# Performance work log

Hardware: AMD Instinct MI355X
Metric: run time of the kernel (lower is better)

The kernel has to match this reference:

```python
import jax, jax.numpy as jnp
import numpy as np

L = 16384      # sequence length
D_IN = 512     # d_input
D_H = 1024     # d_hidden
D_OUT = 512    # d_output
R_MIN = 0.0
R_MAX = 0.99
MAX_PHASE = np.pi


def setup_inputs() -> dict:
    key = jax.random.key(0)
    k_nu, k_th, k_x, k_bre, k_bim, k_cre, k_cim, k_d = jax.random.split(key, 8)
    # nu_init with parametrization='exp'
    u_nu = jax.random.uniform(k_nu, (D_H,), dtype=jnp.float32)
    nu = jnp.sqrt(u_nu * (R_MAX ** 2 - R_MIN ** 2) + R_MIN ** 2)
    u_theta = jax.random.uniform(k_th, (D_H,), dtype=jnp.float32, minval=-MAX_PHASE, maxval=MAX_PHASE)
    theta = jnp.mod(u_theta, 2 * jnp.pi)
    lamb = jnp.stack([jnp.log(-jnp.log(nu)), jnp.log(theta)], axis=0)  # [2, D_H]
    # gamma_init with parametrization='exp': nu = exp(-exp(lamb[0]))
    nu_eff = jnp.exp(-jnp.exp(lamb[0]))
    gamma = jnp.log(jnp.sqrt(1.0 - jnp.abs(nu_eff) ** 2))  # [D_H]
    # matrix_init: normal / sqrt(shape[0])
    B_re = jax.random.normal(k_bre, (D_H, D_IN), dtype=jnp.float32) / jnp.sqrt(D_H)
    B_im = jax.random.normal(k_bim, (D_H, D_IN), dtype=jnp.float32) / jnp.sqrt(D_H)
    C_re = jax.random.normal(k_cre, (D_OUT, D_H), dtype=jnp.float32) / jnp.sqrt(D_OUT)
    C_im = jax.random.normal(k_cim, (D_OUT, D_H), dtype=jnp.float32) / jnp.sqrt(D_OUT)
    D = jax.random.normal(k_d, (D_OUT, D_IN), dtype=jnp.float32) / jnp.sqrt(D_OUT)
    inputs = jax.random.normal(k_x, (L, D_IN), dtype=jnp.float32)
    return {"inputs": inputs, "lamb": lamb, "gamma": gamma,
            "B_re": B_re, "B_im": B_im, "C_re": C_re, "C_im": C_im, "D": D}


def _binary_operator_diag(q_i, q_j):
    A_i, b_i = q_i
    A_j, b_j = q_j
    return (A_j * A_i, A_j * b_i + b_j)


def reference(inputs, lamb, gamma, B_re, B_im, C_re, C_im, D):
    # parametrization='exp': lambda = exp(-exp(nu_log) + i*exp(theta_log))
    diag_lambda = jnp.exp(-jnp.exp(lamb[0]) + 1j * jnp.exp(lamb[1]))  # [D_H] complex64
    # which_gamma='learned', exp param: scale rows of B by exp(gamma)
    B_norm = jnp.exp(gamma)[:, None] * (B_re + 1j * B_im)             # [D_H, D_IN]
    # Bu_t = B_norm @ x_t for all t, as one GEMM: [L, D_H] complex
    Bu = inputs.astype(B_norm.dtype) @ B_norm.T
    Lambda_elements = jnp.broadcast_to(diag_lambda[None, :], Bu.shape)
    # diagonal linear recurrence h_t = lambda*h_{t-1} + Bu_t via parallel scan
    _, h = jax.lax.associative_scan(_binary_operator_diag, (Lambda_elements, Bu))
    C = C_re + 1j * C_im
    # y_t = Re[C h_t] + D x_t
    outputs = jnp.real(h @ C.T) + inputs @ D.T  # [L, D_OUT]
    return outputs
```

## Files before the change

### kernel.cpp

```cpp
#include <hip/hip_runtime.h>

__device__ __forceinline__ unsigned short f2b(float f) {
    unsigned int u = __builtin_bit_cast(unsigned int, f);
    unsigned int r = (u + 0x7FFFu + ((u >> 16) & 1u)) >> 16;
    return (unsigned short)r;
}
__device__ __forceinline__ float b2f(unsigned short s) {
    unsigned int u = ((unsigned int)s) << 16;
    return __builtin_bit_cast(float, u);
}

typedef __attribute__((ext_vector_type(8))) short short8;
typedef __attribute__((ext_vector_type(4))) float float4v;

#define GLD16(g, l) __builtin_amdgcn_global_load_lds(                          \
    (const __attribute__((address_space(1))) unsigned int*)(g),                \
    (__attribute__((address_space(3))) unsigned int*)(l), 16, 0, 0)

#define WAIT_VMN(n)  __builtin_amdgcn_s_waitcnt(0x0F70 | (n))
#define WAIT_LGKM0() __builtin_amdgcn_s_waitcnt(0xC07F)
#define SB()         __builtin_amdgcn_sched_barrier(0)
#define BAR()        __builtin_amdgcn_s_barrier()

#define SEQLEN 16384
#define NCHUNK 512
#define TCHUNK 32
#define LDH 2560

__global__ void prep_all(const float* __restrict__ x,
                         const float* __restrict__ B_re, const float* __restrict__ B_im,
                         const float* __restrict__ gamma,
                         const float* __restrict__ C_re, const float* __restrict__ C_im,
                         const float* __restrict__ Dm,
                         unsigned short* __restrict__ Hcat,
                         unsigned short* __restrict__ Bcat,
                         unsigned short* __restrict__ CW) {
    int b = blockIdx.x;
    if (b < 8192) {
        int id = b * 256 + threadIdx.x;
        int t = id >> 7;
        int k4 = (id & 127) << 2;
        float4 v = *(const float4*)(x + (long)t * 512 + k4);
        ushort4 o;
        o.x = f2b(v.x); o.y = f2b(v.y); o.z = f2b(v.z); o.w = f2b(v.w);
        *(ushort4*)(Hcat + (long)t * LDH + 2048 + k4) = o;
    } else if (b < 9216) {
        int id = (b - 8192) * 256 + threadIdx.x;
        int n = id >> 7;
        int k4 = (id & 127) << 2;
        const float* src = (n < 1024) ? (B_re + (long)n * 512) : (B_im + (long)(n - 1024) * 512);
        float g = expf(gamma[n & 1023]);
        float4 v = *(const float4*)(src + k4);
        ushort4 o;
        o.x = f2b(v.x * g); o.y = f2b(v.y * g); o.z = f2b(v.z * g); o.w = f2b(v.w * g);
        *(ushort4*)(Bcat + (long)n * 512 + k4) = o;
    } else {
        int id = (b - 9216) * 256 + threadIdx.x;
        int o = id / 640;
        int j4 = (id - o * 640) << 2;
        float4 v; float sgn = 1.0f;
        if (j4 < 1024) {
            v = *(const float4*)(C_re + (long)o * 1024 + j4);
        } else if (j4 < 2048) {
            v = *(const float4*)(C_im + (long)o * 1024 + (j4 - 1024));
            sgn = -1.0f;
        } else {
            v = *(const float4*)(Dm + (long)o * 512 + (j4 - 2048));
        }
        ushort4 w;
        w.x = f2b(v.x * sgn); w.y = f2b(v.y * sgn); w.z = f2b(v.z * sgn); w.w = f2b(v.w * sgn);
        *(ushort4*)(CW + (long)o * 2560 + j4) = w;
    }
}

template <int MREP, bool OUT_BF16>
__launch_bounds__(512, 2)
__global__ void gemm_8p(const unsigned short* __restrict__ A, int lda,
                        const unsigned short* __restrict__ B, int ldb,
                        void* __restrict__ Cout, int ldc, int Ktot,
                        int nbx_shift) {
    constexpr int BM  = MREP * 32;
    constexpr int ASH = BM * 64;
    constexpr int NA  = BM / 64;
    constexpr int GPT = NA + 4;
    __shared__ unsigned short sm[2][ASH + 16384] __attribute__((aligned(16)));

    const int tid  = threadIdx.x;
    const int lane = tid & 63;
    const int wid  = tid >> 6;
    const int wr   = wid >> 2;
    const int wc   = wid & 3;

    const int bid = blockIdx.x;
    const int xcd = bid & 7;
    const int g   = bid >> 3;
    const int bx  = g & ((1 << nbx_shift) - 1);
    const int by  = xcd * (gridDim.x >> (3 + nbx_shift)) + (g >> nbx_shift);
    const long m0 = (long)by * BM;
    const long n0 = (long)bx * 256;

    const int sr = lane >> 3;
    const int sc = ((lane & 7) ^ sr) << 3;
    const unsigned short* Agl = A + (m0 + sr) * (long)lda + sc;
    const unsigned short* Bgl = B + (n0 + sr) * (long)ldb + sc;

    const int fr = lane & 15;
    const int x7 = fr & 7;
    const int k0off = (((lane >> 4)    ) ^ x7) << 3;
    const int k1off = (((lane >> 4) + 4) ^ x7) << 3;

    float4v acc[MREP][4] = {};
    short8 fa[4][2];
    short8 fb[4][2];

    auto stageB = [&](unsigned short* buf, long kt) {
        unsigned short* ldsB = buf + ASH + wid * 512;
        const unsigned short* gB = Bgl + kt;
#pragma unroll
        for (int i = 0; i < 4; i++)
            GLD16(gB + (long)(8 * (wid + 8 * i)) * ldb, ldsB + i * 4096);
    };
    auto stageA = [&](unsigned short* buf, long kt) {
        unsigned short* ldsA = buf + wid * 512;
        const unsigned short* gA = Agl + kt;
#pragma unroll
        for (int i = 0; i < NA; i++)
            GLD16(gA + (long)(8 * (wid + 8 * i)) * lda, ldsA + i * 4096);
    };
    auto ldB = [&](const unsigned short* buf, int nbase) {
#pragma unroll
        for (int j = 0; j < 2; j++) {
            const unsigned short* p = buf + ASH + (wc * 64 + (nbase + j) * 16 + fr) * 64;
            fb[nbase + j][0] = *(const short8*)(p + k0off);
            fb[nbase + j][1] = *(const short8*)(p + k1off);
        }
    };

    const int nk = Ktot >> 6;

    stageB(sm[0], 0);  stageA(sm[0], 0);
    stageB(sm[1], 64); stageA(sm[1], 64);
    WAIT_VMN(GPT);
    SB(); BAR(); SB();

    if constexpr (MREP == 8) {
        auto ldA = [&](const unsigned short* buf, int mbase) {
#pragma unroll
            for (int i = 0; i < 4; i++) {
                const unsigned short* p = buf + (wr * 128 + (mbase + i) * 16 + fr) * 64;
                fa[i][0] = *(const short8*)(p + k0off);
                fa[i][1] = *(const short8*)(p + k1off);
            }
        };
        auto mfmaQ = [&](int mbase, int nbase) {
            __builtin_amdgcn_s_setprio(1);
#pragma unroll
            for (int i = 0; i < 4; i++)
#pragma unroll
                for (int j = 0; j < 2; j++) {
                    acc[mbase + i][nbase + j] = __builtin_amdgcn_mfma_f32_16x16x32_bf16(
                        fa[i][0], fb[nbase + j][0], acc[mbase + i][nbase + j], 0, 0, 0);
                    acc[mbase + i][nbase + j] = __builtin_amdgcn_mfma_f32_16x16x32_bf16(
                        fa[i][1], fb[nbase + j][1], acc[mbase + i][nbase + j], 0, 0, 0);
                }
            __builtin_amdgcn_s_setprio(0);
        };
        for (int t = 0; t < nk; ++t) {
            unsigned short* cur = sm[t & 1];
            const bool st = (t + 2 < nk);
            const long kt2 = (long)(t + 2) * 64;
            ldA(cur, 0); ldB(cur, 0);
            SB(); BAR(); SB();
            mfmaQ(0, 0);
            SB(); BAR(); SB();
            ldB(cur, 2);
            SB(); BAR(); SB();
            mfmaQ(0, 2);
            SB(); BAR(); SB();
            if (st) stageB(cur, kt2);
            ldA(cur, 4);
            SB(); BAR(); SB();
            mfmaQ(4, 0);
            SB(); BAR(); SB();
            if (st) stageA(cur, kt2);
            SB();
            mfmaQ(4, 2);
            if (st)              WAIT_VMN(GPT);
            else if (t + 1 < nk) WAIT_VMN(0);
            SB(); BAR(); SB();
        }
    } else {
        auto ldAall = [&](const unsigned short* buf) {
#pragma unroll
            for (int i = 0; i < 4; i++) {
                const unsigned short* p = buf + (wr * 64 + i * 16 + fr) * 64;
                fa[i][0] = *(const short8*)(p + k0off);
                fa[i][1] = *(const short8*)(p + k1off);
            }
        };
        auto mfmaN2 = [&](int nbase) {
            __builtin_amdgcn_s_setprio(1);
#pragma unroll
            for (int i = 0; i < 4; i++)
#pragma unroll
                for (int j = 0; j < 2; j++) {
                    acc[i][nbase + j] = __builtin_amdgcn_mfma_f32_16x16x32_bf16(
                        fa[i][0], fb[nbase + j][0], acc[i][nbase + j], 0, 0, 0);
                    acc[i][nbase + j] = __builtin_amdgcn_mfma_f32_16x16x32_bf16(
                        fa[i][1], fb[nbase + j][1], acc[i][nbase + j], 0, 0, 0);
                }
            __builtin_amdgcn_s_setprio(0);
        };
        for (int t = 0; t < nk; ++t) {
            unsigned short* cur = sm[t & 1];
            const bool st = (t + 2 < nk);
            const long kt2 = (long)(t + 2) * 64;
            ldAall(cur); ldB(cur, 0);
            SB(); BAR(); SB();
            mfmaN2(0);
            SB(); BAR(); SB();
            ldB(cur, 2);
            WAIT_LGKM0();
            SB(); BAR(); SB();
            if (st) { stageB(cur, kt2); stageA(cur, kt2); }
            SB();
            mfmaN2(2);
            if (st)              WAIT_VMN(GPT);
            else if (t + 1 < nk) WAIT_VMN(0);
            SB(); BAR(); SB();
        }
    }

    const int er = (lane >> 4) * 4;
    const int ec = lane & 15;
#pragma unroll
    for (int mi = 0; mi < MREP; mi++) {
#pragma unroll
        for (int r = 0; r < 4; r++) {
            long grow = m0 + wr * (BM / 2) + mi * 16 + er + r;
#pragma unroll
            for (int nj = 0; nj < 4; nj++) {
                long gcol = n0 + wc * 64 + nj * 16 + ec;
                float v = acc[mi][nj][r];
                if (OUT_BF16)
                    ((unsigned short*)Cout)[grow * ldc + gcol] = f2b(v);
                else
                    ((float*)Cout)[grow * ldc + gcol] = v;
            }
        }
    }
}

__global__ void scan_ends(const unsigned short* __restrict__ Hcat,
                          const float* __restrict__ lamb,
                          float* __restrict__ E) {
    const int chunk = blockIdx.x;
    const int ch = threadIdx.x << 2;
    float lre[4], lim[4];
#pragma unroll
    for (int i = 0; i < 4; i++) {
        float nu = expf(-expf(lamb[ch + i]));
        float th = expf(lamb[1024 + ch + i]);
        lre[i] = nu * cosf(th);
        lim[i] = nu * sinf(th);
    }
    float hr[4] = {0, 0, 0, 0}, hi[4] = {0, 0, 0, 0};
    const unsigned short* base = Hcat + (long)chunk * TCHUNK * LDH + ch;
#pragma unroll 4
    for (int t = 0; t < TCHUNK; t++) {
        ushort4 br = *(const ushort4*)(base + (long)t * LDH);
        ushort4 bi = *(const ushort4*)(base + (long)t * LDH + 1024);
        float brf[4] = {b2f(br.x), b2f(br.y), b2f(br.z), b2f(br.w)};
        float bif[4] = {b2f(bi.x), b2f(bi.y), b2f(bi.z), b2f(bi.w)};
#pragma unroll
        for (int i = 0; i < 4; i++) {
            float nr = fmaf(lre[i], hr[i], fmaf(-lim[i], hi[i], brf[i]));
            float ni = fmaf(lre[i], hi[i], fmaf(lim[i], hr[i], bif[i]));
            hr[i] = nr; hi[i] = ni;
        }
    }
    float* Ec = E + (long)chunk * 2048 + ch;
#pragma unroll
    for (int i = 0; i < 4; i++) {
        Ec[i] = hr[i];
        Ec[1024 + i] = hi[i];
    }
}

__global__ void carry(const float* __restrict__ lamb, const float* __restrict__ E,
                      float* __restrict__ Kc) {
    const int lane = threadIdx.x & 63;
    const int ch = blockIdx.x * 4 + (threadIdx.x >> 6);
    double nu = exp(-exp((double)lamb[ch]));
    double th = exp((double)lamb[1024 + ch]);
    double lr = nu * cos(th), li = nu * sin(th);
#pragma unroll
    for (int i = 0; i < 5; i++) {
        double rr = lr * lr - li * li;
        double ii = 2.0 * lr * li;
        lr = rr; li = ii;
    }
    const float tre = (float)lr, tim = (float)li;
    double ar = lr, ai = li;
#pragma unroll
    for (int i = 0; i < 3; i++) {
        double rr = ar * ar - ai * ai;
        double ii = 2.0 * ar * ai;
        ar = rr; ai = ii;
    }
    float Ar = (float)ar, Ai = (float)ai;

    const int c0 = lane * 8;
    float er[8], ei[8];
#pragma unroll
    for (int j = 0; j < 8; j++) {
        er[j] = E[(long)(c0 + j) * 2048 + ch];
        ei[j] = E[(long)(c0 + j) * 2048 + 1024 + ch];
    }
    float hr = 0.0f, hi = 0.0f;
#pragma unroll
    for (int j = 0; j < 8; j++) {
        float nr = fmaf(tre, hr, fmaf(-tim, hi, er[j]));
        float ni = fmaf(tre, hi, fmaf(tim, hr, ei[j]));
        hr = nr; hi = ni;
    }
#pragma unroll
    for (int o = 1; o < 64; o <<= 1) {
        float pr = __shfl_up(hr, o);
        float pi = __shfl_up(hi, o);
        float qr = __shfl_up(Ar, o);
        float qi = __shfl_up(Ai, o);
        if (lane >= o) {
            float nr = fmaf(Ar, pr, fmaf(-Ai, pi, hr));
            float ni = fmaf(Ar, pi, fmaf(Ai, pr, hi));
            hr = nr; hi = ni;
            float nar = Ar * qr - Ai * qi;
            float nai = Ar * qi + Ai * qr;
            Ar = nar; Ai = nai;
        }
    }
    float sr = __shfl_up(hr, 1);
    float si = __shfl_up(hi, 1);
    if (lane == 0) { sr = 0.0f; si = 0.0f; }
#pragma unroll
    for (int j = 0; j < 8; j++) {
        Kc[(long)(c0 + j) * 2048 + ch] = sr;
        Kc[(long)(c0 + j) * 2048 + 1024 + ch] = si;
        float nr = fmaf(tre, sr, fmaf(-tim, si, er[j]));
        float ni = fmaf(tre, si, fmaf(tim, sr, ei[j]));
        sr = nr; si = ni;
    }
}

__global__ void scan_apply(unsigned short* __restrict__ Hcat,
                           const float* __restrict__ lamb,
                           const float* __restrict__ Kc) {
    const int chunk = blockIdx.x;
    const int ch = threadIdx.x << 2;
    float lre[4], lim[4];
#pragma unroll
    for (int i = 0; i < 4; i++) {
        float nu = expf(-expf(lamb[ch + i]));
        float th = expf(lamb[1024 + ch + i]);
        lre[i] = nu * cosf(th);
        lim[i] = nu * sinf(th);
    }
    float hr[4], hi[4];
#pragma unroll
    for (int i = 0; i < 4; i++) {
        hr[i] = Kc[(long)chunk * 2048 + ch + i];
        hi[i] = Kc[(long)chunk * 2048 + 1024 + ch + i];
    }
    unsigned short* base = Hcat + (long)chunk * TCHUNK * LDH + ch;
#pragma unroll 4
    for (int t = 0; t < TCHUNK; t++) {
        ushort4 br = *(const ushort4*)(base + (long)t * LDH);
        ushort4 bi = *(const ushort4*)(base + (long)t * LDH + 1024);
        float brf[4] = {b2f(br.x), b2f(br.y), b2f(br.z), b2f(br.w)};
        float bif[4] = {b2f(bi.x), b2f(bi.y), b2f(bi.z), b2f(bi.w)};
#pragma unroll
        for (int i = 0; i < 4; i++) {
            float nr = fmaf(lre[i], hr[i], fmaf(-lim[i], hi[i], brf[i]));
            float ni = fmaf(lre[i], hi[i], fmaf(lim[i], hr[i], bif[i]));
            hr[i] = nr; hi[i] = ni;
        }
        ushort4 orv, oiv;
        orv.x = f2b(hr[0]); orv.y = f2b(hr[1]); orv.z = f2b(hr[2]); orv.w = f2b(hr[3]);
        oiv.x = f2b(hi[0]); oiv.y = f2b(hi[1]); oiv.z = f2b(hi[2]); oiv.w = f2b(hi[3]);
        *(ushort4*)(base + (long)t * LDH) = orv;
        *(ushort4*)(base + (long)t * LDH + 1024) = oiv;
    }
}

extern "C" void kernel_launch(void* const* d_in, const int* in_sizes, int n_in,
                              void* d_out, int out_size, void* d_ws, size_t ws_size,
                              hipStream_t stream) {
    const float* x     = (const float*)d_in[0];
    const float* lamb  = (const float*)d_in[1];
    const float* gamma = (const float*)d_in[2];
    const float* B_re  = (const float*)d_in[3];
    const float* B_im  = (const float*)d_in[4];
    const float* C_re  = (const float*)d_in[5];
    const float* C_im  = (const float*)d_in[6];
    const float* Dm    = (const float*)d_in[7];

    char* ws = (char*)d_ws;
    unsigned short* Hcat = (unsigned short*)ws;
    float* E  = (float*)(ws + 83886080);
    float* Kc = E + (long)NCHUNK * 2048;
    unsigned short* Bcat = (unsigned short*)((char*)Kc + 4194304);
    unsigned short* CW   = Bcat + (long)2048 * 512;

    prep_all<<<10496, 256, 0, stream>>>(x, B_re, B_im, gamma, C_re, C_im, Dm, Hcat, Bcat, CW);
    gemm_8p<8, true><<<512, 512, 0, stream>>>(Hcat + 2048, LDH, Bcat, 512, Hcat, LDH, 512,
                                              3);
    scan_ends<<<NCHUNK, 256, 0, stream>>>(Hcat, lamb, E);
    carry<<<256, 256, 0, stream>>>(lamb, E, Kc);
    scan_apply<<<NCHUNK, 256, 0, stream>>>(Hcat, lamb, Kc);
    gemm_8p<4, false><<<256, 512, 0, stream>>>(Hcat, LDH, CW, 2560, (float*)d_out, 512, 2560,
                                               1);
}
```

Before: 242.1 us.

## Replace 8-wave GEMM with 4-wave 256x128 tile, K=32 triple-buffered pipeline

Replaces the templated 8-wave GEMM with a single 4-wave kernel that uses 256x128 output tiles, a K step of 32, and three rotating LDS buffers with a new XOR swizzle. Both GEMMs now launch with 256 threads: the first on 1024 blocks and the second on 256 blocks with 256x128 tiles. The aim is a deeper prefetch pipeline and more MFMA work per wave with fewer barriers per tile. In exchange, each K iteration is shorter, so barriers are relatively more frequent. The output GEMM also gets fewer waves in total, which may leave the device underfilled.

```diff
diff --git a/kernel.cpp b/kernel.cpp
--- a/kernel.cpp
+++ b/kernel.cpp
@@ -18,7 +18,6 @@
     (__attribute__((address_space(3))) unsigned int*)(l), 16, 0, 0)
 
 #define WAIT_VMN(n)  __builtin_amdgcn_s_waitcnt(0x0F70 | (n))
-#define WAIT_LGKM0() __builtin_amdgcn_s_waitcnt(0xC07F)
 #define SB()         __builtin_amdgcn_sched_barrier(0)
 #define BAR()        __builtin_amdgcn_s_barrier()
 
@@ -73,171 +72,100 @@
     }
 }
 
-template <int MREP, bool OUT_BF16>
-__launch_bounds__(512, 2)
-__global__ void gemm_8p(const unsigned short* __restrict__ A, int lda,
+template <bool OUT_BF16>
+__launch_bounds__(256, 2)
+__global__ void gemm_w4(const unsigned short* __restrict__ A, int lda,
                         const unsigned short* __restrict__ B, int ldb,
                         void* __restrict__ Cout, int ldc, int Ktot,
                         int nbx_shift) {
-    constexpr int BM  = MREP * 32;
-    constexpr int ASH = BM * 64;
-    constexpr int NA  = BM / 64;
-    constexpr int GPT = NA + 4;
-    __shared__ unsigned short sm[2][ASH + 16384] __attribute__((aligned(16)));
-
+    __shared__ unsigned short sm[3][12288] __attribute__((aligned(16)));
     const int tid  = threadIdx.x;
     const int lane = tid & 63;
     const int wid  = tid >> 6;
-    const int wr   = wid >> 2;
-    const int wc   = wid & 3;
+    const int wr   = wid >> 1;
+    const int wc   = wid & 1;
 
     const int bid = blockIdx.x;
     const int xcd = bid & 7;
     const int g   = bid >> 3;
     const int bx  = g & ((1 << nbx_shift) - 1);
     const int by  = xcd * (gridDim.x >> (3 + nbx_shift)) + (g >> nbx_shift);
-    const long m0 = (long)by * BM;
-    const long n0 = (long)bx * 256;
-
-    const int sr = lane >> 3;
-    const int sc = ((lane & 7) ^ sr) << 3;
+    const long m0 = (long)by * 256;
+    const long n0 = (long)bx * 128;
+
+    const int sr = lane >> 2;
+    const int sc = (((lane & 3) ^ ((lane >> 3) & 3)) << 3);
     const unsigned short* Agl = A + (m0 + sr) * (long)lda + sc;
     const unsigned short* Bgl = B + (n0 + sr) * (long)ldb + sc;
 
-    const int fr = lane & 15;
-    const int x7 = fr & 7;
-    const int k0off = (((lane >> 4)    ) ^ x7) << 3;
-    const int k1off = (((lane >> 4) + 4) ^ x7) << 3;
-
-    float4v acc[MREP][4] = {};
-    short8 fa[4][2];
-    short8 fb[4][2];
-
-    auto stageB = [&](unsigned short* buf, long kt) {
-        unsigned short* ldsB = buf + ASH + wid * 512;
-        const unsigned short* gB = Bgl + kt;
+    const int fr   = lane & 15;
+    const int koff = (((lane >> 4) ^ ((fr >> 1) & 3)) << 3);
+
+    float4v acc[8][4] = {};
+    short8 fa[8], fb[4];
+
+    auto stage = [&](unsigned short* buf, long kt) {
 #pragma unroll
         for (int i = 0; i < 4; i++)
-            GLD16(gB + (long)(8 * (wid + 8 * i)) * ldb, ldsB + i * 4096);
+            GLD16(Agl + (long)(wid * 64 + i * 16) * lda + kt, buf + (wid * 4 + i) * 512);
+#pragma unroll
+        for (int j = 0; j < 2; j++)
+            GLD16(Bgl + (long)(wid * 32 + j * 16) * ldb + kt, buf + 8192 + (wid * 2 + j) * 512);
     };
-    auto stageA = [&](unsigned short* buf, long kt) {
-        unsigned short* ldsA = buf + wid * 512;
-        const unsigned short* gA = Agl + kt;
-#pragma unroll
-        for (int i = 0; i < NA; i++)
-            GLD16(gA + (long)(8 * (wid + 8 * i)) * lda, ldsA + i * 4096);
+    auto ldAall = [&](const unsigned short* buf) {
+#pragma unroll
+        for (int i = 0; i < 8; i++)
+            fa[i] = *(const short8*)(buf + (wr * 128 + i * 16 + fr) * 32 + koff);
     };
-    auto ldB = [&](const unsigned short* buf, int nbase) {
-#pragma unroll
-        for (int j = 0; j < 2; j++) {
-            const unsigned short* p = buf + ASH + (wc * 64 + (nbase + j) * 16 + fr) * 64;
-            fb[nbase + j][0] = *(const short8*)(p + k0off);
-            fb[nbase + j][1] = *(const short8*)(p + k1off);
-        }
+    auto ldB2 = [&](const unsigned short* buf, int nbase) {
+#pragma unroll
+        for (int j = 0; j < 2; j++)
+            fb[nbase + j] = *(const short8*)(buf + 8192 + (wc * 64 + (nbase + j) * 16 + fr) * 32 + koff);
     };
-
-    const int nk = Ktot >> 6;
-
-    stageB(sm[0], 0);  stageA(sm[0], 0);
-    stageB(sm[1], 64); stageA(sm[1], 64);
-    WAIT_VMN(GPT);
+    auto mfma16 = [&](int nbase) {
+        __builtin_amdgcn_s_setprio(1);
+#pragma unroll
+        for (int i = 0; i < 8; i++)
+#pragma unroll
+            for (int j = 0; j < 2; j++)
+                acc[i][nbase + j] = __builtin_amdgcn_mfma_f32_16x16x32_bf16(
+                    fa[i], fb[nbase + j], acc[i][nbase + j], 0, 0, 0);
+        __builtin_amdgcn_s_setprio(0);
+    };
+
+    const int nk = Ktot >> 5;
+
+    unsigned short* p0 = sm[0];
+    unsigned short* p1 = sm[1];
+    unsigned short* p2 = sm[2];
+    stage(p0, 0);
+    stage(p1, 32);
+    WAIT_VMN(6);
     SB(); BAR(); SB();
 
-    if constexpr (MREP == 8) {
-        auto ldA = [&](const unsigned short* buf, int mbase) {
-#pragma unroll
-            for (int i = 0; i < 4; i++) {
-                const unsigned short* p = buf + (wr * 128 + (mbase + i) * 16 + fr) * 64;
-                fa[i][0] = *(const short8*)(p + k0off);
-                fa[i][1] = *(const short8*)(p + k1off);
-            }
-        };
-        auto mfmaQ = [&](int mbase, int nbase) {
-            __builtin_amdgcn_s_setprio(1);
-#pragma unroll
-            for (int i = 0; i < 4; i++)
-#pragma unroll
-                for (int j = 0; j < 2; j++) {
-                    acc[mbase + i][nbase + j] = __builtin_amdgcn_mfma_f32_16x16x32_bf16(
-                        fa[i][0], fb[nbase + j][0], acc[mbase + i][nbase + j], 0, 0, 0);
-                    acc[mbase + i][nbase + j] = __builtin_amdgcn_mfma_f32_16x16x32_bf16(
-                        fa[i][1], fb[nbase + j][1], acc[mbase + i][nbase + j], 0, 0, 0);
-                }
-            __builtin_amdgcn_s_setprio(0);
-        };
-        for (int t = 0; t < nk; ++t) {
-            unsigned short* cur = sm[t & 1];
-            const bool st = (t + 2 < nk);
-            const long kt2 = (long)(t + 2) * 64;
-            ldA(cur, 0); ldB(cur, 0);
-            SB(); BAR(); SB();
-            mfmaQ(0, 0);
-            SB(); BAR(); SB();
-            ldB(cur, 2);
-            SB(); BAR(); SB();
-            mfmaQ(0, 2);
-            SB(); BAR(); SB();
-            if (st) stageB(cur, kt2);
-            ldA(cur, 4);
-            SB(); BAR(); SB();
-            mfmaQ(4, 0);
-            SB(); BAR(); SB();
-            if (st) stageA(cur, kt2);
-            SB();
-            mfmaQ(4, 2);
-            if (st)              WAIT_VMN(GPT);
-            else if (t + 1 < nk) WAIT_VMN(0);
-            SB(); BAR(); SB();
-        }
-    } else {
-        auto ldAall = [&](const unsigned short* buf) {
-#pragma unroll
-            for (int i = 0; i < 4; i++) {
-                const unsigned short* p = buf + (wr * 64 + i * 16 + fr) * 64;
-                fa[i][0] = *(const short8*)(p + k0off);
-                fa[i][1] = *(const short8*)(p + k1off);
-            }
-        };
-        auto mfmaN2 = [&](int nbase) {
-            __builtin_amdgcn_s_setprio(1);
-#pragma unroll
-            for (int i = 0; i < 4; i++)
-#pragma unroll
-                for (int j = 0; j < 2; j++) {
-                    acc[i][nbase + j] = __builtin_amdgcn_mfma_f32_16x16x32_bf16(
-                        fa[i][0], fb[nbase + j][0], acc[i][nbase + j], 0, 0, 0);
-                    acc[i][nbase + j] = __builtin_amdgcn_mfma_f32_16x16x32_bf16(
-                        fa[i][1], fb[nbase + j][1], acc[i][nbase + j], 0, 0, 0);
-                }
-            __builtin_amdgcn_s_setprio(0);
-        };
-        for (int t = 0; t < nk; ++t) {
-            unsigned short* cur = sm[t & 1];
-            const bool st = (t + 2 < nk);
-            const long kt2 = (long)(t + 2) * 64;
-            ldAall(cur); ldB(cur, 0);
-            SB(); BAR(); SB();
-            mfmaN2(0);
-            SB(); BAR(); SB();
-            ldB(cur, 2);
-            WAIT_LGKM0();
-            SB(); BAR(); SB();
-            if (st) { stageB(cur, kt2); stageA(cur, kt2); }
-            SB();
-            mfmaN2(2);
-            if (st)              WAIT_VMN(GPT);
-            else if (t + 1 < nk) WAIT_VMN(0);
-            SB(); BAR(); SB();
-        }
+    for (int t = 0; t < nk; ++t) {
+        const bool st = (t + 2 < nk);
+        ldAall(p0); ldB2(p0, 0);
+        SB(); BAR(); SB();
+        mfma16(0);
+        SB(); BAR(); SB();
+        ldB2(p0, 2);
+        if (st) stage(p2, (long)(t + 2) * 32);
+        SB(); BAR(); SB();
+        mfma16(2);
+        if (st)              WAIT_VMN(6);
+        else if (t + 1 < nk) WAIT_VMN(0);
+        SB(); BAR(); SB();
+        unsigned short* tmp = p0; p0 = p1; p1 = p2; p2 = tmp;
     }
 
     const int er = (lane >> 4) * 4;
     const int ec = lane & 15;
 #pragma unroll
-    for (int mi = 0; mi < MREP; mi++) {
+    for (int mi = 0; mi < 8; mi++) {
 #pragma unroll
         for (int r = 0; r < 4; r++) {
-            long grow = m0 + wr * (BM / 2) + mi * 16 + er + r;
+            long grow = m0 + wr * 128 + mi * 16 + er + r;
 #pragma unroll
             for (int nj = 0; nj < 4; nj++) {
                 long gcol = n0 + wc * 64 + nj * 16 + ec;
@@ -412,11 +340,11 @@
     unsigned short* CW   = Bcat + (long)2048 * 512;
 
     prep_all<<<10496, 256, 0, stream>>>(x, B_re, B_im, gamma, C_re, C_im, Dm, Hcat, Bcat, CW);
-    gemm_8p<8, true><<<512, 512, 0, stream>>>(Hcat + 2048, LDH, Bcat, 512, Hcat, LDH, 512,
-                                              3);
+    gemm_w4<true><<<1024, 256, 0, stream>>>(Hcat + 2048, LDH, Bcat, 512, Hcat, LDH, 512,
+                                            4);
     scan_ends<<<NCHUNK, 256, 0, stream>>>(Hcat, lamb, E);
     carry<<<256, 256, 0, stream>>>(lamb, E, Kc);
     scan_apply<<<NCHUNK, 256, 0, stream>>>(Hcat, lamb, Kc);
-    gemm_8p<4, false><<<256, 512, 0, stream>>>(Hcat, LDH, CW, 2560, (float*)d_out, 512, 2560,
-                                               1);
-}
+    gemm_w4<false><<<256, 256, 0, stream>>>(Hcat, LDH, CW, 2560, (float*)d_out, 512, 2560,
+                                            2);
+}
```

Result: no change. 243.3 us (+0.5%).

## Use split-K with atomic accumulation for output GEMM and unify 256x256 tiles

Applied to the files above, without the earlier changes.

The output GEMM (K=2560) now uses 256x256 tiles with the K dimension split in two halves. Partial results are accumulated with float atomicAdd into an output buffer that prep_all zeroes in extra blocks. This keeps the same 256-block count but uses larger, more reuse-efficient tiles. Both GEMMs share one body with launch bounds lowered to one block per CU. The atomic adds and the extra zeroing pass are added costs, and the accumulation order becomes nondeterministic.

```diff
diff --git a/kernel.cpp b/kernel.cpp
--- a/kernel.cpp
+++ b/kernel.cpp
@@ -18,7 +18,6 @@
     (__attribute__((address_space(3))) unsigned int*)(l), 16, 0, 0)
 
 #define WAIT_VMN(n)  __builtin_amdgcn_s_waitcnt(0x0F70 | (n))
-#define WAIT_LGKM0() __builtin_amdgcn_s_waitcnt(0xC07F)
 #define SB()         __builtin_amdgcn_sched_barrier(0)
 #define BAR()        __builtin_amdgcn_s_barrier()
 
@@ -34,7 +33,8 @@
                          const float* __restrict__ Dm,
                          unsigned short* __restrict__ Hcat,
                          unsigned short* __restrict__ Bcat,
-                         unsigned short* __restrict__ CW) {
+                         unsigned short* __restrict__ CW,
+                         float* __restrict__ Yzero) {
     int b = blockIdx.x;
     if (b < 8192) {
         int id = b * 256 + threadIdx.x;
@@ -54,7 +54,7 @@
         ushort4 o;
         o.x = f2b(v.x * g); o.y = f2b(v.y * g); o.z = f2b(v.z * g); o.w = f2b(v.w * g);
         *(ushort4*)(Bcat + (long)n * 512 + k4) = o;
-    } else {
+    } else if (b < 10496) {
         int id = (b - 9216) * 256 + threadIdx.x;
         int o = id / 640;
         int j4 = (id - o * 640) << 2;
@@ -70,20 +70,21 @@
         ushort4 w;
         w.x = f2b(v.x * sgn); w.y = f2b(v.y * sgn); w.z = f2b(v.z * sgn); w.w = f2b(v.w * sgn);
         *(ushort4*)(CW + (long)o * 2560 + j4) = w;
-    }
-}
-
-template <int MREP, bool OUT_BF16>
-__launch_bounds__(512, 2)
-__global__ void gemm_8p(const unsigned short* __restrict__ A, int lda,
-                        const unsigned short* __restrict__ B, int ldb,
-                        void* __restrict__ Cout, int ldc, int Ktot,
-                        int nbx_shift) {
-    constexpr int BM  = MREP * 32;
-    constexpr int ASH = BM * 64;
-    constexpr int NA  = BM / 64;
-    constexpr int GPT = NA + 4;
-    __shared__ unsigned short sm[2][ASH + 16384] __attribute__((aligned(16)));
+    } else {
+        int id = (b - 10496) * 256 + threadIdx.x;
+        float4 z = {0.0f, 0.0f, 0.0f, 0.0f};
+        *(float4*)(Yzero + (long)id * 4) = z;
+    }
+}
+
+template <int EPI>
+__device__ __forceinline__ void gemm256_body(
+        const unsigned short* __restrict__ A, int lda,
+        const unsigned short* __restrict__ B, int ldb,
+        void* __restrict__ Cout, int ldc,
+        int nk, long kbase, long m0, long n0) {
+    constexpr int ASH = 16384;
+    __shared__ unsigned short sm[2][32768] __attribute__((aligned(16)));
 
     const int tid  = threadIdx.x;
     const int lane = tid & 63;
@@ -91,25 +92,17 @@
     const int wr   = wid >> 2;
     const int wc   = wid & 3;
 
-    const int bid = blockIdx.x;
-    const int xcd = bid & 7;
-    const int g   = bid >> 3;
-    const int bx  = g & ((1 << nbx_shift) - 1);
-    const int by  = xcd * (gridDim.x >> (3 + nbx_shift)) + (g >> nbx_shift);
-    const long m0 = (long)by * BM;
-    const long n0 = (long)bx * 256;
-
     const int sr = lane >> 3;
     const int sc = ((lane & 7) ^ sr) << 3;
-    const unsigned short* Agl = A + (m0 + sr) * (long)lda + sc;
-    const unsigned short* Bgl = B + (n0 + sr) * (long)ldb + sc;
+    const unsigned short* Agl = A + (m0 + sr) * (long)lda + sc + kbase;
+    const unsigned short* Bgl = B + (n0 + sr) * (long)ldb + sc + kbase;
 
     const int fr = lane & 15;
     const int x7 = fr & 7;
     const int k0off = (((lane >> 4)    ) ^ x7) << 3;
     const int k1off = (((lane >> 4) + 4) ^ x7) << 3;
 
-    float4v acc[MREP][4] = {};
+    float4v acc[8][4] = {};
     short8 fa[4][2];
     short8 fb[4][2];
 
@@ -124,8 +117,16 @@
         unsigned short* ldsA = buf + wid * 512;
         const unsigned short* gA = Agl + kt;
 #pragma unroll
-        for (int i = 0; i < NA; i++)
+        for (int i = 0; i < 4; i++)
             GLD16(gA + (long)(8 * (wid + 8 * i)) * lda, ldsA + i * 4096);
+    };
+    auto ldA = [&](const unsigned short* buf, int mbase) {
+#pragma unroll
+        for (int i = 0; i < 4; i++) {
+            const unsigned short* p = buf + (wr * 128 + (mbase + i) * 16 + fr) * 64;
+            fa[i][0] = *(const short8*)(p + k0off);
+            fa[i][1] = *(const short8*)(p + k1off);
+        }
     };
     auto ldB = [&](const unsigned short* buf, int nbase) {
 #pragma unroll
@@ -135,120 +136,91 @@
             fb[nbase + j][1] = *(const short8*)(p + k1off);
         }
     };
-
-    const int nk = Ktot >> 6;
+    auto mfmaQ = [&](int mbase, int nbase) {
+        __builtin_amdgcn_s_setprio(1);
+#pragma unroll
+        for (int i = 0; i < 4; i++)
+#pragma unroll
+            for (int j = 0; j < 2; j++) {
+                acc[mbase + i][nbase + j] = __builtin_amdgcn_mfma_f32_16x16x32_bf16(
+                    fa[i][0], fb[nbase + j][0], acc[mbase + i][nbase + j], 0, 0, 0);
+                acc[mbase + i][nbase + j] = __builtin_amdgcn_mfma_f32_16x16x32_bf16(
+                    fa[i][1], fb[nbase + j][1], acc[mbase + i][nbase + j], 0, 0, 0);
+            }
+        __builtin_amdgcn_s_setprio(0);
+    };
 
     stageB(sm[0], 0);  stageA(sm[0], 0);
     stageB(sm[1], 64); stageA(sm[1], 64);
-    WAIT_VMN(GPT);
+    WAIT_VMN(8);
     SB(); BAR(); SB();
 
-    if constexpr (MREP == 8) {
-        auto ldA = [&](const unsigned short* buf, int mbase) {
-#pragma unroll
-            for (int i = 0; i < 4; i++) {
-                const unsigned short* p = buf + (wr * 128 + (mbase + i) * 16 + fr) * 64;
-                fa[i][0] = *(const short8*)(p + k0off);
-                fa[i][1] = *(const short8*)(p + k1off);
-            }
-        };
-        auto mfmaQ = [&](int mbase, int nbase) {
-            __builtin_amdgcn_s_setprio(1);
-#pragma unroll
-            for (int i = 0; i < 4; i++)
-#pragma unroll
-                for (int j = 0; j < 2; j++) {
-                    acc[mbase + i][nbase + j] = __builtin_amdgcn_mfma_f32_16x16x32_bf16(
-                        fa[i][0], fb[nbase + j][0], acc[mbase + i][nbase + j], 0, 0, 0);
-                    acc[mbase + i][nbase + j] = __builtin_amdgcn_mfma_f32_16x16x32_bf16(
-                        fa[i][1], fb[nbase + j][1], acc[mbase + i][nbase + j], 0, 0, 0);
-                }
-            __builtin_amdgcn_s_setprio(0);
-        };
-        for (int t = 0; t < nk; ++t) {
-            unsigned short* cur = sm[t & 1];
-            const bool st = (t + 2 < nk);
-            const long kt2 = (long)(t + 2) * 64;
-            ldA(cur, 0); ldB(cur, 0);
-            SB(); BAR(); SB();
-            mfmaQ(0, 0);
-            SB(); BAR(); SB();
-            ldB(cur, 2);
-            SB(); BAR(); SB();
-            mfmaQ(0, 2);
-            SB(); BAR(); SB();
-            if (st) stageB(cur, kt2);
-            ldA(cur, 4);
-            SB(); BAR(); SB();
-            mfmaQ(4, 0);
-            SB(); BAR(); SB();
-            if (st) stageA(cur, kt2);
-            SB();
-            mfmaQ(4, 2);
-            if (st)              WAIT_VMN(GPT);
-            else if (t + 1 < nk) WAIT_VMN(0);
-            SB(); BAR(); SB();
-        }
-    } else {
-        auto ldAall = [&](const unsigned short* buf) {
-#pragma unroll
-            for (int i = 0; i < 4; i++) {
-                const unsigned short* p = buf + (wr * 64 + i * 16 + fr) * 64;
-                fa[i][0] = *(const short8*)(p + k0off);
-                fa[i][1] = *(const short8*)(p + k1off);
-            }
-        };
-        auto mfmaN2 = [&](int nbase) {
-            __builtin_amdgcn_s_setprio(1);
-#pragma unroll
-            for (int i = 0; i < 4; i++)
-#pragma unroll
-                for (int j = 0; j < 2; j++) {
-                    acc[i][nbase + j] = __builtin_amdgcn_mfma_f32_16x16x32_bf16(
-                        fa[i][0], fb[nbase + j][0], acc[i][nbase + j], 0, 0, 0);
-                    acc[i][nbase + j] = __builtin_amdgcn_mfma_f32_16x16x32_bf16(
-                        fa[i][1], fb[nbase + j][1], acc[i][nbase + j], 0, 0, 0);
-                }
-            __builtin_amdgcn_s_setprio(0);
-        };
-        for (int t = 0; t < nk; ++t) {
-            unsigned short* cur = sm[t & 1];
-            const bool st = (t + 2 < nk);
-            const long kt2 = (long)(t + 2) * 64;
-            ldAall(cur); ldB(cur, 0);
-            SB(); BAR(); SB();
-            mfmaN2(0);
-            SB(); BAR(); SB();
-            ldB(cur, 2);
-            WAIT_LGKM0();
-            SB(); BAR(); SB();
-            if (st) { stageB(cur, kt2); stageA(cur, kt2); }
-            SB();
-            mfmaN2(2);
-            if (st)              WAIT_VMN(GPT);
-            else if (t + 1 < nk) WAIT_VMN(0);
-            SB(); BAR(); SB();
-        }
+    for (int t = 0; t < nk; ++t) {
+        unsigned short* cur = sm[t & 1];
+        const bool st = (t + 2 < nk);
+        const long kt2 = (long)(t + 2) * 64;
+        ldA(cur, 0); ldB(cur, 0);
+        SB(); BAR(); SB();
+        mfmaQ(0, 0);
+        SB(); BAR(); SB();
+        ldB(cur, 2);
+        SB(); BAR(); SB();
+        mfmaQ(0, 2);
+        SB(); BAR(); SB();
+        if (st) stageB(cur, kt2);
+        ldA(cur, 4);
+        SB(); BAR(); SB();
+        mfmaQ(4, 0);
+        SB(); BAR(); SB();
+        if (st) stageA(cur, kt2);
+        SB();
+        mfmaQ(4, 2);
+        if (st)              WAIT_VMN(8);
+        else if (t + 1 < nk) WAIT_VMN(0);
+        SB(); BAR(); SB();
     }
 
     const int er = (lane >> 4) * 4;
     const int ec = lane & 15;
 #pragma unroll
-    for (int mi = 0; mi < MREP; mi++) {
+    for (int mi = 0; mi < 8; mi++) {
 #pragma unroll
         for (int r = 0; r < 4; r++) {
-            long grow = m0 + wr * (BM / 2) + mi * 16 + er + r;
+            long grow = m0 + wr * 128 + mi * 16 + er + r;
 #pragma unroll
             for (int nj = 0; nj < 4; nj++) {
                 long gcol = n0 + wc * 64 + nj * 16 + ec;
                 float v = acc[mi][nj][r];
-                if (OUT_BF16)
+                if (EPI == 0)
                     ((unsigned short*)Cout)[grow * ldc + gcol] = f2b(v);
                 else
-                    ((float*)Cout)[grow * ldc + gcol] = v;
+                    atomicAdd(&((float*)Cout)[grow * ldc + gcol], v);
             }
         }
     }
+}
+
+__global__ __launch_bounds__(512, 1)
+void gemm_bu(const unsigned short* __restrict__ A, int lda,
+             const unsigned short* __restrict__ B, int ldb,
+             void* __restrict__ Cout, int ldc) {
+    const int bid = blockIdx.x;
+    const int l = (bid & 7) * 64 + (bid >> 3);
+    const long m0 = (long)(l >> 3) * 256;
+    const long n0 = (long)(l & 7) * 256;
+    gemm256_body<0>(A, lda, B, ldb, Cout, ldc, 8, 0, m0, n0);
+}
+
+__global__ __launch_bounds__(512, 1)
+void gemm_y(const unsigned short* __restrict__ A, int lda,
+            const unsigned short* __restrict__ B, int ldb,
+            void* __restrict__ Cout, int ldc) {
+    const int bid = blockIdx.x;
+    const int l = (bid & 7) * 32 + (bid >> 3);
+    const long kbase = (long)(l & 1) * 1280;
+    const long n0 = (long)((l >> 1) & 1) * 256;
+    const long m0 = (long)(l >> 2) * 256;
+    gemm256_body<1>(A, lda, B, ldb, Cout, ldc, 20, kbase, m0, n0);
 }
 
 __global__ void scan_ends(const unsigned short* __restrict__ Hcat,
@@ -411,12 +383,11 @@
     unsigned short* Bcat = (unsigned short*)((char*)Kc + 4194304);
     unsigned short* CW   = Bcat + (long)2048 * 512;
 
-    prep_all<<<10496, 256, 0, stream>>>(x, B_re, B_im, gamma, C_re, C_im, Dm, Hcat, Bcat, CW);
-    gemm_8p<8, true><<<512, 512, 0, stream>>>(Hcat + 2048, LDH, Bcat, 512, Hcat, LDH, 512,
-                                              3);
+    prep_all<<<12544, 256, 0, stream>>>(x, B_re, B_im, gamma, C_re, C_im, Dm,
+                                        Hcat, Bcat, CW, (float*)d_out);
+    gemm_bu<<<512, 512, 0, stream>>>(Hcat + 2048, LDH, Bcat, 512, Hcat, LDH);
     scan_ends<<<NCHUNK, 256, 0, stream>>>(Hcat, lamb, E);
     carry<<<256, 256, 0, stream>>>(lamb, E, Kc);
     scan_apply<<<NCHUNK, 256, 0, stream>>>(Hcat, lamb, Kc);
-    gemm_8p<4, false><<<256, 512, 0, stream>>>(Hcat, LDH, CW, 2560, (float*)d_out, 512, 2560,
-                                               1);
-}
+    gemm_y<<<256, 512, 0, stream>>>(Hcat, LDH, CW, 2560, (float*)d_out, 512);
+}
```

Measured after the change: 274.8 us. 1.13x slower.
